# Kernel tuning notes

Measured on AMD Instinct MI355X. Metric: run time of the kernel, lower is better.

## Reference

```python
import jax, jax.numpy as jnp
import numpy as np

B, S, E, H = 2, 2048, 768, 12
D = E // H  # head_dim = 64


def setup_inputs() -> dict:
    key = jax.random.key(0)
    ks = jax.random.split(key, 5)
    scale = 1.0 / np.sqrt(E)
    return {
        "x": jax.random.normal(ks[0], (B, S, E), dtype=jnp.float32),
        "Wq": jax.random.normal(ks[1], (E, E), dtype=jnp.float32) * scale,
        "bq": jnp.zeros((E,), dtype=jnp.float32),
        "Wk": jax.random.normal(ks[2], (E, E), dtype=jnp.float32) * scale,
        "bk": jnp.zeros((E,), dtype=jnp.float32),
        "Wv": jax.random.normal(ks[3], (E, E), dtype=jnp.float32) * scale,
        "bv": jnp.zeros((E,), dtype=jnp.float32),
        "Wo": jax.random.normal(ks[4], (E, E), dtype=jnp.float32) * scale,
        "bo": jnp.zeros((E,), dtype=jnp.float32),
    }


def reference(x, Wq, bq, Wk, bk, Wv, bv, Wo, bo):
    # Linear layers (torch nn.Linear: y = x @ W^T + b; here W stored as (E,E), use x @ W + b)
    q = (x @ Wq + bq).reshape(B, S, H, D).transpose(0, 2, 1, 3)  # (B,H,S,D)
    k = (x @ Wk + bk).reshape(B, S, H, D).transpose(0, 2, 1, 3)
    v = (x @ Wv + bv).reshape(B, S, H, D).transpose(0, 2, 1, 3)
    scores = jnp.einsum("bhqd,bhkd->bhqk", q, k) / jnp.sqrt(jnp.float32(D))
    weights = jax.nn.softmax(scores, axis=-1)  # (B,H,S,S) -- explicitly returned
    out = jnp.einsum("bhqk,bhkd->bhqd", weights, v)
    out = out.transpose(0, 2, 1, 3).reshape(B, S, E)
    output = out @ Wo + bo
    return (output, weights)
```

## Files before the change

### kernel.cpp

```cpp
#include <hip/hip_runtime.h>
#include <hip/hip_fp16.h>

#define B_ 2
#define S_ 2048
#define E_ 768
#define H_ 12
#define D_ 64
#define BS_ 4096

typedef _Float16 half8 __attribute__((ext_vector_type(8)));
typedef _Float16 half4 __attribute__((ext_vector_type(4)));
typedef float f32x4 __attribute__((ext_vector_type(4)));

__device__ __forceinline__ f32x4 mfma16(half8 a, half8 b, f32x4 c) {
    return __builtin_amdgcn_mfma_f32_16x16x32_f16(a, b, c, 0, 0, 0);
}

__device__ __forceinline__ void gll16(const void* g, void* s) {
    __builtin_amdgcn_global_load_lds((const __attribute__((address_space(1))) void*)g,
                                     (__attribute__((address_space(3))) void*)s, 16, 0, 0);
}

__global__ void cast_x_kernel(const float* __restrict__ x, _Float16* __restrict__ xh, int n) {
    int i = (blockIdx.x * blockDim.x + threadIdx.x) * 4;
    if (i < n) {
        float4 v = *reinterpret_cast<const float4*>(x + i);
        half4 o;
        o.x = (_Float16)v.x; o.y = (_Float16)v.y; o.z = (_Float16)v.z; o.w = (_Float16)v.w;
        *reinterpret_cast<half4*>(xh + i) = o;
    }
}

__global__ void transpose_w_kernel(const float* __restrict__ W0, const float* __restrict__ W1,
                                   const float* __restrict__ W2, const float* __restrict__ W3,
                                   _Float16* __restrict__ Wt) {
    __shared__ float tile[32][33];
    int mat = blockIdx.z;
    const float* W = (mat == 0) ? W0 : (mat == 1) ? W1 : (mat == 2) ? W2 : W3;
    _Float16* dst = Wt + (size_t)mat * E_ * E_;
    int out0 = blockIdx.x * 32, in0 = blockIdx.y * 32;
    int tx = threadIdx.x & 31, ty = threadIdx.x >> 5;
    #pragma unroll
    for (int r = ty; r < 32; r += 8) tile[r][tx] = W[(size_t)(in0 + r) * E_ + out0 + tx];
    __syncthreads();
    #pragma unroll
    for (int r = ty; r < 32; r += 8) dst[(size_t)(out0 + r) * E_ + in0 + tx] = (_Float16)tile[tx][r];
}

__global__ __launch_bounds__(256) void qkv_kernel(const _Float16* __restrict__ xh,
                                                  const _Float16* __restrict__ Wt,
                                                  const float* __restrict__ bq, const float* __restrict__ bk,
                                                  const float* __restrict__ bv,
                                                  _Float16* __restrict__ qw, _Float16* __restrict__ kw,
                                                  _Float16* __restrict__ vT) {
    __shared__ __align__(16) _Float16 ldsA[2][128 * 32];
    __shared__ __align__(16) _Float16 ldsB[2][64 * 32];
    int n0 = blockIdx.x * 64;
    int m0 = blockIdx.y * 128;
    int mat = n0 / E_;
    int col0 = n0 - mat * E_;
    int tid = threadIdx.x;
    int lane = tid & 63, wv = tid >> 6;
    int l15 = lane & 15, lhi = lane >> 4;
    int wm = wv >> 1, wn = wv & 1;
    const _Float16* Wm = Wt + (size_t)mat * E_ * E_ + (size_t)col0 * E_;
    const _Float16* Am = xh + (size_t)m0 * E_;

    int srowA = wv * 16 + (lane >> 2);
    int sc16  = lane & 3;

    auto stage = [&](int buf, int k0) {
        #pragma unroll
        for (int is = 0; is < 2; ++is) {
            int row = is * 64 + srowA;
            const char* src = (const char*)(Am + (size_t)row * E_ + k0) + ((sc16 ^ ((row >> 1) & 3)) << 4);
            gll16(src, &ldsA[buf][is * 2048 + wv * 512]);
        }
        {
            int row = srowA;
            const char* src = (const char*)(Wm + (size_t)row * E_ + k0) + ((sc16 ^ ((row >> 1) & 3)) << 4);
            gll16(src, &ldsB[buf][wv * 512]);
        }
    };

    f32x4 acc[4][2];
    #pragma unroll
    for (int mi = 0; mi < 4; ++mi)
        #pragma unroll
        for (int nj = 0; nj < 2; ++nj) acc[mi][nj] = (f32x4){0.f, 0.f, 0.f, 0.f};

    stage(0, 0);
    __syncthreads();
    for (int t = 0; t < E_ / 32; ++t) {
        if (t + 1 < E_ / 32) stage((t + 1) & 1, (t + 1) * 32);
        const _Float16* At = ldsA[t & 1];
        const _Float16* Bt = ldsB[t & 1];
        half8 af[4], bf[2];
        #pragma unroll
        for (int mi = 0; mi < 4; ++mi) {
            int row = wm * 64 + mi * 16 + l15;
            af[mi] = *reinterpret_cast<const half8*>(At + row * 32 + ((lhi ^ ((row >> 1) & 3)) << 3));
        }
        #pragma unroll
        for (int nj = 0; nj < 2; ++nj) {
            int row = wn * 32 + nj * 16 + l15;
            bf[nj] = *reinterpret_cast<const half8*>(Bt + row * 32 + ((lhi ^ ((row >> 1) & 3)) << 3));
        }
        #pragma unroll
        for (int mi = 0; mi < 4; ++mi)
            #pragma unroll
            for (int nj = 0; nj < 2; ++nj) acc[mi][nj] = mfma16(af[mi], bf[nj], acc[mi][nj]);
        __syncthreads();
    }

    const float* bias = (mat == 0) ? bq : (mat == 1) ? bk : bv;
    #pragma unroll
    for (int nj = 0; nj < 2; ++nj) {
        int col = col0 + wn * 32 + nj * 16 + l15;
        int h = col >> 6, d = col & 63;
        float bsv = bias[col];
        #pragma unroll
        for (int mi = 0; mi < 4; ++mi) {
            #pragma unroll
            for (int r = 0; r < 4; ++r) {
                int token = m0 + wm * 64 + mi * 16 + lhi * 4 + r;
                int bb = token >> 11, s = token & (S_ - 1);
                _Float16 val = (_Float16)(acc[mi][nj][r] + bsv);
                if (mat == 0)      qw[(((size_t)bb * H_ + h) * S_ + s) * D_ + d] = val;
                else if (mat == 1) kw[(((size_t)bb * H_ + h) * S_ + s) * D_ + d] = val;
                else               vT[(((size_t)bb * H_ + h) * D_ + d) * S_ + s] = val;
            }
        }
    }
}

__global__ __launch_bounds__(256) void attn_kernel(const _Float16* __restrict__ qw,
                                                   const _Float16* __restrict__ kw,
                                                   const _Float16* __restrict__ vT,
                                                   float* __restrict__ wout,
                                                   _Float16* __restrict__ aout) {
    __shared__ __align__(16) _Float16 ldsK[2][64 * 64];
    __shared__ __align__(16) _Float16 ldsV[2][64 * 64];
    __shared__ __align__(16) _Float16 plds[4][16 * 64];
    int qt = blockIdx.x, h = blockIdx.y, bb = blockIdx.z;
    int tid = threadIdx.x;
    int lane = tid & 63, w = tid >> 6;
    int l15 = lane & 15, lhi = lane >> 4;
    int q0 = qt * 64 + 16 * w;
    size_t bh = (size_t)bb * H_ + h;
    const _Float16* qbase = qw + bh * S_ * D_;
    const _Float16* kbase = kw + bh * S_ * D_;
    const _Float16* vbase = vT + bh * D_ * S_;

    int srow = w * 8 + (lane >> 3);
    int sc16 = lane & 7;

    auto stageK = [&](int buf, int kt0) {
        #pragma unroll
        for (int is = 0; is < 2; ++is) {
            int row = is * 32 + srow;
            const char* src = (const char*)(kbase + (size_t)(kt0 + row) * D_) + ((sc16 ^ (row & 7)) << 4);
            gll16(src, &ldsK[buf][is * 2048 + w * 512]);
        }
    };
    auto stageV = [&](int buf, int kt0) {
        #pragma unroll
        for (int is = 0; is < 2; ++is) {
            int row = is * 32 + srow;
            const char* src = (const char*)(vbase + (size_t)row * S_ + kt0) + ((sc16 ^ (row & 7)) << 4);
            gll16(src, &ldsV[buf][is * 2048 + w * 512]);
        }
    };

    half8 qa[2];
    #pragma unroll
    for (int kf = 0; kf < 2; ++kf)
        qa[kf] = *reinterpret_cast<const half8*>(qbase + (size_t)(q0 + l15) * D_ + kf * 32 + lhi * 8);

    float lsum[4] = {0.f, 0.f, 0.f, 0.f};
    stageK(0, 0);
    __syncthreads();
    for (int kt = 0; kt < S_ / 64; ++kt) {
        if (kt + 1 < S_ / 64) stageK((kt + 1) & 1, (kt + 1) * 64);
        const _Float16* Kb = ldsK[kt & 1];
        #pragma unroll
        for (int nf = 0; nf < 4; ++nf) {
            f32x4 sacc = (f32x4){0.f, 0.f, 0.f, 0.f};
            int row = nf * 16 + l15;
            #pragma unroll
            for (int kf = 0; kf < 2; ++kf) {
                half8 kb = *reinterpret_cast<const half8*>(Kb + row * 64 + (((kf * 4 + lhi) ^ (row & 7)) << 3));
                sacc = mfma16(qa[kf], kb, sacc);
            }
            #pragma unroll
            for (int r = 0; r < 4; ++r) lsum[r] += __expf(sacc[r] * 0.125f);
        }
        __syncthreads();
    }
    #pragma unroll
    for (int r = 0; r < 4; ++r) {
        float v = lsum[r];
        v += __shfl_xor(v, 1);
        v += __shfl_xor(v, 2);
        v += __shfl_xor(v, 4);
        v += __shfl_xor(v, 8);
        lsum[r] = 1.0f / v;
    }

    f32x4 oacc[4];
    #pragma unroll
    for (int df = 0; df < 4; ++df) oacc[df] = (f32x4){0.f, 0.f, 0.f, 0.f};
    float* wbase = wout + bh * (size_t)S_ * S_;

    stageK(0, 0);
    stageV(0, 0);
    __syncthreads();
    for (int kt = 0; kt < S_ / 64; ++kt) {
        if (kt + 1 < S_ / 64) { stageK((kt + 1) & 1, (kt + 1) * 64); stageV((kt + 1) & 1, (kt + 1) * 64); }
        const _Float16* Kb = ldsK[kt & 1];
        const _Float16* Vb = ldsV[kt & 1];
        #pragma unroll
        for (int nf = 0; nf < 4; ++nf) {
            f32x4 sacc = (f32x4){0.f, 0.f, 0.f, 0.f};
            int row = nf * 16 + l15;
            #pragma unroll
            for (int kf = 0; kf < 2; ++kf) {
                half8 kb = *reinterpret_cast<const half8*>(Kb + row * 64 + (((kf * 4 + lhi) ^ (row & 7)) << 3));
                sacc = mfma16(qa[kf], kb, sacc);
            }
            #pragma unroll
            for (int r = 0; r < 4; ++r) {
                float p = __expf(sacc[r] * 0.125f) * lsum[r];
                int q = lhi * 4 + r;
                int k = nf * 16 + l15;
                __builtin_nontemporal_store(p, &wbase[(size_t)(q0 + q) * S_ + kt * 64 + k]);
                plds[w][q * 64 + (((k >> 3) ^ (q & 7)) << 3) + (k & 7)] = (_Float16)p;
            }
        }
        #pragma unroll
        for (int ks = 0; ks < 2; ++ks) {
            half8 pa = *reinterpret_cast<const half8*>(&plds[w][l15 * 64 + (((ks * 4 + lhi) ^ (l15 & 7)) << 3)]);
            #pragma unroll
            for (int df = 0; df < 4; ++df) {
                int drow = df * 16 + l15;
                half8 vb = *reinterpret_cast<const half8*>(Vb + drow * 64 + (((ks * 4 + lhi) ^ (drow & 7)) << 3));
                oacc[df] = mfma16(pa, vb, oacc[df]);
            }
        }
        __syncthreads();
    }

    #pragma unroll
    for (int df = 0; df < 4; ++df) {
        #pragma unroll
        for (int r = 0; r < 4; ++r) {
            int token = bb * S_ + q0 + lhi * 4 + r;
            aout[(size_t)token * E_ + h * D_ + df * 16 + l15] = (_Float16)(oacc[df][r]);
        }
    }
}

__global__ __launch_bounds__(256) void proj_kernel(const _Float16* __restrict__ ah,
                                                   const _Float16* __restrict__ Wto,
                                                   const float* __restrict__ bo,
                                                   float* __restrict__ out) {
    __shared__ __align__(16) _Float16 ldsA[2][128 * 32];
    __shared__ __align__(16) _Float16 ldsB[2][64 * 32];
    int n0 = blockIdx.x * 64;
    int m0 = blockIdx.y * 128;
    int tid = threadIdx.x;
    int lane = tid & 63, wv = tid >> 6;
    int l15 = lane & 15, lhi = lane >> 4;
    int wm = wv >> 1, wn = wv & 1;
    const _Float16* Am = ah + (size_t)m0 * E_;
    const _Float16* Bm = Wto + (size_t)n0 * E_;

    int srowA = wv * 16 + (lane >> 2);
    int sc16  = lane & 3;

    auto stage = [&](int buf, int k0) {
        #pragma unroll
        for (int is = 0; is < 2; ++is) {
            int row = is * 64 + srowA;
            const char* src = (const char*)(Am + (size_t)row * E_ + k0) + ((sc16 ^ ((row >> 1) & 3)) << 4);
            gll16(src, &ldsA[buf][is * 2048 + wv * 512]);
        }
        {
            int row = srowA;
            const char* src = (const char*)(Bm + (size_t)row * E_ + k0) + ((sc16 ^ ((row >> 1) & 3)) << 4);
            gll16(src, &ldsB[buf][wv * 512]);
        }
    };

    f32x4 acc[4][2];
    #pragma unroll
    for (int mi = 0; mi < 4; ++mi)
        #pragma unroll
        for (int nj = 0; nj < 2; ++nj) acc[mi][nj] = (f32x4){0.f, 0.f, 0.f, 0.f};

    stage(0, 0);
    __syncthreads();
    for (int t = 0; t < E_ / 32; ++t) {
        if (t + 1 < E_ / 32) stage((t + 1) & 1, (t + 1) * 32);
        const _Float16* At = ldsA[t & 1];
        const _Float16* Bt = ldsB[t & 1];
        half8 af[4], bf[2];
        #pragma unroll
        for (int mi = 0; mi < 4; ++mi) {
            int row = wm * 64 + mi * 16 + l15;
            af[mi] = *reinterpret_cast<const half8*>(At + row * 32 + ((lhi ^ ((row >> 1) & 3)) << 3));
        }
        #pragma unroll
        for (int nj = 0; nj < 2; ++nj) {
            int row = wn * 32 + nj * 16 + l15;
            bf[nj] = *reinterpret_cast<const half8*>(Bt + row * 32 + ((lhi ^ ((row >> 1) & 3)) << 3));
        }
        #pragma unroll
        for (int mi = 0; mi < 4; ++mi)
            #pragma unroll
            for (int nj = 0; nj < 2; ++nj) acc[mi][nj] = mfma16(af[mi], bf[nj], acc[mi][nj]);
        __syncthreads();
    }

    #pragma unroll
    for (int nj = 0; nj < 2; ++nj) {
        int col = n0 + wn * 32 + nj * 16 + l15;
        float bsv = bo[col];
        #pragma unroll
        for (int mi = 0; mi < 4; ++mi) {
            #pragma unroll
            for (int r = 0; r < 4; ++r) {
                int token = m0 + wm * 64 + mi * 16 + lhi * 4 + r;
                out[(size_t)token * E_ + col] = acc[mi][nj][r] + bsv;
            }
        }
    }
}

extern "C" void kernel_launch(void* const* d_in, const int* in_sizes, int n_in,
                              void* d_out, int out_size, void* d_ws, size_t ws_size,
                              hipStream_t stream) {
    const float* x  = (const float*)d_in[0];
    const float* Wq = (const float*)d_in[1];
    const float* bq = (const float*)d_in[2];
    const float* Wk = (const float*)d_in[3];
    const float* bk = (const float*)d_in[4];
    const float* Wv = (const float*)d_in[5];
    const float* bv = (const float*)d_in[6];
    const float* Wo = (const float*)d_in[7];
    const float* bo = (const float*)d_in[8];

    char* ws = (char*)d_ws;
    _Float16* xh   = (_Float16*)(ws);
    _Float16* Wt   = (_Float16*)(ws + 6291456);
    _Float16* qw   = (_Float16*)(ws + 11010048);
    _Float16* kw   = (_Float16*)(ws + 17301504);
    _Float16* vT   = (_Float16*)(ws + 23592960);
    _Float16* aout = (_Float16*)(ws + 29884416);
    (void)ws_size; (void)in_sizes; (void)n_in; (void)out_size;

    float* out  = (float*)d_out;
    float* wout = out + (size_t)BS_ * E_;

    cast_x_kernel<<<dim3(BS_ * E_ / 1024), dim3(256), 0, stream>>>(x, xh, BS_ * E_);
    transpose_w_kernel<<<dim3(E_ / 32, E_ / 32, 4), dim3(256), 0, stream>>>(Wq, Wk, Wv, Wo, Wt);
    qkv_kernel<<<dim3(3 * E_ / 64, BS_ / 128), dim3(256), 0, stream>>>(xh, Wt, bq, bk, bv, qw, kw, vT);
    attn_kernel<<<dim3(S_ / 64, H_, B_), dim3(256), 0, stream>>>(qw, kw, vT, wout, aout);
    proj_kernel<<<dim3(E_ / 64, BS_ / 128), dim3(256), 0, stream>>>(aout, Wt + (size_t)3 * E_ * E_, bo, out);
}
```

Measured before the change: 235.8 us.

## Fuse prep kernels, widen GEMM tiles, use exp2 and setprio in attention

Merges the x-cast and weight-transpose kernels into one launch and doubles the N tile of the QKV and output-projection GEMMs to 128, for more MFMA reuse per LDS load. In attention, exp becomes exp2 with the scale pre-folded into one constant, and s_setprio is raised around the MFMA sections. The projection output uses nontemporal stores. Larger tiles halve the grid, which risks underfilling the CUs for the small projection GEMM.

```diff
diff --git a/kernel.cpp b/kernel.cpp
--- a/kernel.cpp
+++ b/kernel.cpp
@@ -12,6 +12,8 @@
 typedef _Float16 half4 __attribute__((ext_vector_type(4)));
 typedef float f32x4 __attribute__((ext_vector_type(4)));
 
+#define EXP_C 0.18033688011112042f
+
 __device__ __forceinline__ f32x4 mfma16(half8 a, half8 b, f32x4 c) {
     return __builtin_amdgcn_mfma_f32_16x16x32_f16(a, b, c, 0, 0, 0);
 }
@@ -21,23 +23,25 @@
                                      (__attribute__((address_space(3))) void*)s, 16, 0, 0);
 }
 
-__global__ void cast_x_kernel(const float* __restrict__ x, _Float16* __restrict__ xh, int n) {
-    int i = (blockIdx.x * blockDim.x + threadIdx.x) * 4;
-    if (i < n) {
-        float4 v = *reinterpret_cast<const float4*>(x + i);
-        half4 o;
-        o.x = (_Float16)v.x; o.y = (_Float16)v.y; o.z = (_Float16)v.z; o.w = (_Float16)v.w;
-        *reinterpret_cast<half4*>(xh + i) = o;
-    }
-}
-
-__global__ void transpose_w_kernel(const float* __restrict__ W0, const float* __restrict__ W1,
-                                   const float* __restrict__ W2, const float* __restrict__ W3,
-                                   _Float16* __restrict__ Wt) {
+__global__ void prep_kernel(const float* __restrict__ x,
+                            const float* __restrict__ W0, const float* __restrict__ W1,
+                            const float* __restrict__ W2, const float* __restrict__ W3,
+                            _Float16* __restrict__ Wt, _Float16* __restrict__ xh) {
+    int z = blockIdx.z;
+    if (z == 4) {
+        int n = BS_ * E_;
+        int stride = 24 * 24 * 256 * 4;
+        for (int i = ((blockIdx.y * 24 + blockIdx.x) * 256 + threadIdx.x) * 4; i < n; i += stride) {
+            float4 v = *reinterpret_cast<const float4*>(x + i);
+            half4 o;
+            o.x = (_Float16)v.x; o.y = (_Float16)v.y; o.z = (_Float16)v.z; o.w = (_Float16)v.w;
+            *reinterpret_cast<half4*>(xh + i) = o;
+        }
+        return;
+    }
     __shared__ float tile[32][33];
-    int mat = blockIdx.z;
-    const float* W = (mat == 0) ? W0 : (mat == 1) ? W1 : (mat == 2) ? W2 : W3;
-    _Float16* dst = Wt + (size_t)mat * E_ * E_;
+    const float* W = (z == 0) ? W0 : (z == 1) ? W1 : (z == 2) ? W2 : W3;
+    _Float16* dst = Wt + (size_t)z * E_ * E_;
     int out0 = blockIdx.x * 32, in0 = blockIdx.y * 32;
     int tx = threadIdx.x & 31, ty = threadIdx.x >> 5;
     #pragma unroll
@@ -54,8 +58,8 @@
                                                   _Float16* __restrict__ qw, _Float16* __restrict__ kw,
                                                   _Float16* __restrict__ vT) {
     __shared__ __align__(16) _Float16 ldsA[2][128 * 32];
-    __shared__ __align__(16) _Float16 ldsB[2][64 * 32];
-    int n0 = blockIdx.x * 64;
+    __shared__ __align__(16) _Float16 ldsB[2][128 * 32];
+    int n0 = blockIdx.x * 128;
     int m0 = blockIdx.y * 128;
     int mat = n0 / E_;
     int col0 = n0 - mat * E_;
@@ -63,31 +67,27 @@
     int lane = tid & 63, wv = tid >> 6;
     int l15 = lane & 15, lhi = lane >> 4;
     int wm = wv >> 1, wn = wv & 1;
-    const _Float16* Wm = Wt + (size_t)mat * E_ * E_ + (size_t)col0 * E_;
     const _Float16* Am = xh + (size_t)m0 * E_;
-
-    int srowA = wv * 16 + (lane >> 2);
-    int sc16  = lane & 3;
+    const _Float16* Bm = Wt + (size_t)mat * E_ * E_ + (size_t)col0 * E_;
+
+    int srow = wv * 16 + (lane >> 2);
+    int sc16 = lane & 3;
 
     auto stage = [&](int buf, int k0) {
         #pragma unroll
         for (int is = 0; is < 2; ++is) {
-            int row = is * 64 + srowA;
-            const char* src = (const char*)(Am + (size_t)row * E_ + k0) + ((sc16 ^ ((row >> 1) & 3)) << 4);
-            gll16(src, &ldsA[buf][is * 2048 + wv * 512]);
-        }
-        {
-            int row = srowA;
-            const char* src = (const char*)(Wm + (size_t)row * E_ + k0) + ((sc16 ^ ((row >> 1) & 3)) << 4);
-            gll16(src, &ldsB[buf][wv * 512]);
+            int row = is * 64 + srow;
+            int c = (sc16 ^ ((row >> 1) & 3)) << 4;
+            gll16((const char*)(Am + (size_t)row * E_ + k0) + c, &ldsA[buf][is * 2048 + wv * 512]);
+            gll16((const char*)(Bm + (size_t)row * E_ + k0) + c, &ldsB[buf][is * 2048 + wv * 512]);
         }
     };
 
-    f32x4 acc[4][2];
+    f32x4 acc[4][4];
     #pragma unroll
     for (int mi = 0; mi < 4; ++mi)
         #pragma unroll
-        for (int nj = 0; nj < 2; ++nj) acc[mi][nj] = (f32x4){0.f, 0.f, 0.f, 0.f};
+        for (int nj = 0; nj < 4; ++nj) acc[mi][nj] = (f32x4){0.f, 0.f, 0.f, 0.f};
 
     stage(0, 0);
     __syncthreads();
@@ -95,28 +95,28 @@
         if (t + 1 < E_ / 32) stage((t + 1) & 1, (t + 1) * 32);
         const _Float16* At = ldsA[t & 1];
         const _Float16* Bt = ldsB[t & 1];
-        half8 af[4], bf[2];
+        half8 af[4], bf[4];
         #pragma unroll
         for (int mi = 0; mi < 4; ++mi) {
             int row = wm * 64 + mi * 16 + l15;
             af[mi] = *reinterpret_cast<const half8*>(At + row * 32 + ((lhi ^ ((row >> 1) & 3)) << 3));
         }
         #pragma unroll
-        for (int nj = 0; nj < 2; ++nj) {
-            int row = wn * 32 + nj * 16 + l15;
+        for (int nj = 0; nj < 4; ++nj) {
+            int row = wn * 64 + nj * 16 + l15;
             bf[nj] = *reinterpret_cast<const half8*>(Bt + row * 32 + ((lhi ^ ((row >> 1) & 3)) << 3));
         }
         #pragma unroll
         for (int mi = 0; mi < 4; ++mi)
             #pragma unroll
-            for (int nj = 0; nj < 2; ++nj) acc[mi][nj] = mfma16(af[mi], bf[nj], acc[mi][nj]);
+            for (int nj = 0; nj < 4; ++nj) acc[mi][nj] = mfma16(af[mi], bf[nj], acc[mi][nj]);
         __syncthreads();
     }
 
     const float* bias = (mat == 0) ? bq : (mat == 1) ? bk : bv;
     #pragma unroll
-    for (int nj = 0; nj < 2; ++nj) {
-        int col = col0 + wn * 32 + nj * 16 + l15;
+    for (int nj = 0; nj < 4; ++nj) {
+        int col = col0 + wn * 64 + nj * 16 + l15;
         int h = col >> 6, d = col & 63;
         float bsv = bias[col];
         #pragma unroll
@@ -187,13 +187,15 @@
         for (int nf = 0; nf < 4; ++nf) {
             f32x4 sacc = (f32x4){0.f, 0.f, 0.f, 0.f};
             int row = nf * 16 + l15;
+            __builtin_amdgcn_s_setprio(1);
             #pragma unroll
             for (int kf = 0; kf < 2; ++kf) {
                 half8 kb = *reinterpret_cast<const half8*>(Kb + row * 64 + (((kf * 4 + lhi) ^ (row & 7)) << 3));
                 sacc = mfma16(qa[kf], kb, sacc);
             }
-            #pragma unroll
-            for (int r = 0; r < 4; ++r) lsum[r] += __expf(sacc[r] * 0.125f);
+            __builtin_amdgcn_s_setprio(0);
+            #pragma unroll
+            for (int r = 0; r < 4; ++r) lsum[r] += exp2f(sacc[r] * EXP_C);
         }
         __syncthreads();
     }
@@ -223,20 +225,23 @@
         for (int nf = 0; nf < 4; ++nf) {
             f32x4 sacc = (f32x4){0.f, 0.f, 0.f, 0.f};
             int row = nf * 16 + l15;
+            __builtin_amdgcn_s_setprio(1);
             #pragma unroll
             for (int kf = 0; kf < 2; ++kf) {
                 half8 kb = *reinterpret_cast<const half8*>(Kb + row * 64 + (((kf * 4 + lhi) ^ (row & 7)) << 3));
                 sacc = mfma16(qa[kf], kb, sacc);
             }
+            __builtin_amdgcn_s_setprio(0);
             #pragma unroll
             for (int r = 0; r < 4; ++r) {
-                float p = __expf(sacc[r] * 0.125f) * lsum[r];
+                float p = exp2f(sacc[r] * EXP_C) * lsum[r];
                 int q = lhi * 4 + r;
                 int k = nf * 16 + l15;
                 __builtin_nontemporal_store(p, &wbase[(size_t)(q0 + q) * S_ + kt * 64 + k]);
                 plds[w][q * 64 + (((k >> 3) ^ (q & 7)) << 3) + (k & 7)] = (_Float16)p;
             }
         }
+        __builtin_amdgcn_s_setprio(1);
         #pragma unroll
         for (int ks = 0; ks < 2; ++ks) {
             half8 pa = *reinterpret_cast<const half8*>(&plds[w][l15 * 64 + (((ks * 4 + lhi) ^ (l15 & 7)) << 3)]);
@@ -247,6 +252,7 @@
                 oacc[df] = mfma16(pa, vb, oacc[df]);
             }
         }
+        __builtin_amdgcn_s_setprio(0);
         __syncthreads();
     }
 
@@ -265,8 +271,8 @@
                                                    const float* __restrict__ bo,
                                                    float* __restrict__ out) {
     __shared__ __align__(16) _Float16 ldsA[2][128 * 32];
-    __shared__ __align__(16) _Float16 ldsB[2][64 * 32];
-    int n0 = blockIdx.x * 64;
+    __shared__ __align__(16) _Float16 ldsB[2][128 * 32];
+    int n0 = blockIdx.x * 128;
     int m0 = blockIdx.y * 128;
     int tid = threadIdx.x;
     int lane = tid & 63, wv = tid >> 6;
@@ -275,28 +281,24 @@
     const _Float16* Am = ah + (size_t)m0 * E_;
     const _Float16* Bm = Wto + (size_t)n0 * E_;
 
-    int srowA = wv * 16 + (lane >> 2);
-    int sc16  = lane & 3;
+    int srow = wv * 16 + (lane >> 2);
+    int sc16 = lane & 3;
 
     auto stage = [&](int buf, int k0) {
         #pragma unroll
         for (int is = 0; is < 2; ++is) {
-            int row = is * 64 + srowA;
-            const char* src = (const char*)(Am + (size_t)row * E_ + k0) + ((sc16 ^ ((row >> 1) & 3)) << 4);
-            gll16(src, &ldsA[buf][is * 2048 + wv * 512]);
-        }
-        {
-            int row = srowA;
-            const char* src = (const char*)(Bm + (size_t)row * E_ + k0) + ((sc16 ^ ((row >> 1) & 3)) << 4);
-            gll16(src, &ldsB[buf][wv * 512]);
+            int row = is * 64 + srow;
+            int c = (sc16 ^ ((row >> 1) & 3)) << 4;
+            gll16((const char*)(Am + (size_t)row * E_ + k0) + c, &ldsA[buf][is * 2048 + wv * 512]);
+            gll16((const char*)(Bm + (size_t)row * E_ + k0) + c, &ldsB[buf][is * 2048 + wv * 512]);
         }
     };
 
-    f32x4 acc[4][2];
+    f32x4 acc[4][4];
     #pragma unroll
     for (int mi = 0; mi < 4; ++mi)
         #pragma unroll
-        for (int nj = 0; nj < 2; ++nj) acc[mi][nj] = (f32x4){0.f, 0.f, 0.f, 0.f};
+        for (int nj = 0; nj < 4; ++nj) acc[mi][nj] = (f32x4){0.f, 0.f, 0.f, 0.f};
 
     stage(0, 0);
     __syncthreads();
@@ -304,34 +306,34 @@
         if (t + 1 < E_ / 32) stage((t + 1) & 1, (t + 1) * 32);
         const _Float16* At = ldsA[t & 1];
         const _Float16* Bt = ldsB[t & 1];
-        half8 af[4], bf[2];
+        half8 af[4], bf[4];
         #pragma unroll
         for (int mi = 0; mi < 4; ++mi) {
             int row = wm * 64 + mi * 16 + l15;
             af[mi] = *reinterpret_cast<const half8*>(At + row * 32 + ((lhi ^ ((row >> 1) & 3)) << 3));
         }
         #pragma unroll
-        for (int nj = 0; nj < 2; ++nj) {
-            int row = wn * 32 + nj * 16 + l15;
+        for (int nj = 0; nj < 4; ++nj) {
+            int row = wn * 64 + nj * 16 + l15;
             bf[nj] = *reinterpret_cast<const half8*>(Bt + row * 32 + ((lhi ^ ((row >> 1) & 3)) << 3));
         }
         #pragma unroll
         for (int mi = 0; mi < 4; ++mi)
             #pragma unroll
-            for (int nj = 0; nj < 2; ++nj) acc[mi][nj] = mfma16(af[mi], bf[nj], acc[mi][nj]);
+            for (int nj = 0; nj < 4; ++nj) acc[mi][nj] = mfma16(af[mi], bf[nj], acc[mi][nj]);
         __syncthreads();
     }
 
     #pragma unroll
-    for (int nj = 0; nj < 2; ++nj) {
-        int col = n0 + wn * 32 + nj * 16 + l15;
+    for (int nj = 0; nj < 4; ++nj) {
+        int col = n0 + wn * 64 + nj * 16 + l15;
         float bsv = bo[col];
         #pragma unroll
         for (int mi = 0; mi < 4; ++mi) {
             #pragma unroll
             for (int r = 0; r < 4; ++r) {
                 int token = m0 + wm * 64 + mi * 16 + lhi * 4 + r;
-                out[(size_t)token * E_ + col] = acc[mi][nj][r] + bsv;
+                __builtin_nontemporal_store(acc[mi][nj][r] + bsv, &out[(size_t)token * E_ + col]);
             }
         }
     }
@@ -362,9 +364,8 @@
     float* out  = (float*)d_out;
     float* wout = out + (size_t)BS_ * E_;
 
-    cast_x_kernel<<<dim3(BS_ * E_ / 1024), dim3(256), 0, stream>>>(x, xh, BS_ * E_);
-    transpose_w_kernel<<<dim3(E_ / 32, E_ / 32, 4), dim3(256), 0, stream>>>(Wq, Wk, Wv, Wo, Wt);
-    qkv_kernel<<<dim3(3 * E_ / 64, BS_ / 128), dim3(256), 0, stream>>>(xh, Wt, bq, bk, bv, qw, kw, vT);
+    prep_kernel<<<dim3(24, 24, 5), dim3(256), 0, stream>>>(x, Wq, Wk, Wv, Wo, Wt, xh);
+    qkv_kernel<<<dim3(3 * E_ / 128, BS_ / 128), dim3(256), 0, stream>>>(xh, Wt, bq, bk, bv, qw, kw, vT);
     attn_kernel<<<dim3(S_ / 64, H_, B_), dim3(256), 0, stream>>>(qw, kw, vT, wout, aout);
-    proj_kernel<<<dim3(E_ / 64, BS_ / 128), dim3(256), 0, stream>>>(aout, Wt + (size_t)3 * E_ * E_, bo, out);
-}
+    proj_kernel<<<dim3(E_ / 128, BS_ / 128), dim3(256), 0, stream>>>(aout, Wt + (size_t)3 * E_ * E_, bo, out);
+}
```

After: 237.4 us. About the same (+0.7%).
